# Kernel optimization log

Hardware: AMD Instinct MI355X
Metric: run time of the kernel (lower is better)

The kernel has to match this reference:

```python
import jax, jax.numpy as jnp
import numpy as np
from jax import lax

IN_CH = 64
OUT_CH = 64
K = 3
CW = 2 * IN_CH + 49  # in_ch_weight = 2*in_ch + MAX_DISPLACEMENT**2 = 177
B = 8


def setup_inputs() -> dict:
    key = jax.random.key(0)
    ks = jax.random.split(key, 14)
    f = lambda k, s, sc: jax.random.normal(k, s, dtype=jnp.float32) * sc
    he5 = lambda cin: (2.0 / (cin * 25)) ** 0.5
    he3 = lambda cin: (2.0 / (cin * 9)) ** 0.5
    return {
        "x0": f(ks[0], (B, IN_CH, 128, 160), 1.0),
        "y0": f(ks[1], (B, IN_CH, 128, 160), 1.0),
        "x": f(ks[2], (B, IN_CH, 64, 80), 1.0),
        "y": f(ks[3], (B, IN_CH, 64, 80), 1.0),
        # weight-branch 0 (outputs CW channels)
        "w1a": f(ks[4], (IN_CH, CW, 5, 5), he5(CW)),
        "w1b": f(ks[5], (IN_CH, IN_CH, 5, 5), he5(IN_CH)),
        "w1c": f(ks[6], (CW, IN_CH, 3, 3), he3(IN_CH)),
        # weight-branch 1 / final (outputs OUT_CH channels)
        "w2a": f(ks[7], (IN_CH, CW, 5, 5), he5(CW)),
        "w2b": f(ks[8], (IN_CH, IN_CH, 5, 5), he5(IN_CH)),
        "w2c": f(ks[9], (OUT_CH, IN_CH, 3, 3), he3(IN_CH)),
        # grouped 1x1 dynamic-weight generators (per-channel affine maps)
        "wx_w": f(ks[10], (CW, CW * K * K), 0.05),
        "wx_b": f(ks[11], (CW, CW * K * K), 0.05),
        "wxf_w": f(ks[12], (OUT_CH, OUT_CH * K * K), 0.05),
        "wxf_b": f(ks[13], (OUT_CH, OUT_CH * K * K), 0.05),
    }


def _conv(x, w, stride, pad):
    return lax.conv_general_dilated(
        x, w, (stride, stride), [(pad, pad), (pad, pad)],
        dimension_numbers=("NCHW", "OIHW", "NCHW"))


def _pool2(x):
    b, c, h, w = x.shape
    return x.reshape(b, c, h // 2, 2, w // 2, 2).mean(axis=(3, 5))


def _corr(x0, y0):
    # FlowNet-style correlation: max_displacement=7, stride2=2 ->
    # displacements {-6,-4,-2,0,2,4,6}^2 = 49 channels; mean over C.
    b, c, h, w = x0.shape
    D = 6
    yp = jnp.pad(y0, ((0, 0), (0, 0), (D, D), (D, D)))
    outs = []
    for dy in range(-6, 7, 2):
        for dx in range(-6, 7, 2):
            ys = yp[:, :, D + dy:D + dy + h, D + dx:D + dx + w]
            outs.append(jnp.mean(x0 * ys, axis=1))
    return jnp.stack(outs, axis=1)  # [B, 49, H, W]


def _branch(feat, wa, wb, wc):
    h = jax.nn.relu(_conv(feat, wa, 2, 2))
    h = jax.nn.relu(_conv(h, wb, 2, 2))
    h = _conv(h, wc, 2, 1)
    return h.mean(axis=(2, 3))  # adaptive_avg_pool2d -> (1,1), squeezed: [B, Cout]


def _adaptive_conv(x, w, pad):
    # per-sample conv weights w: [B, Cout, Cin, k, k]
    def one(xb, wb):
        return _conv(xb[None], wb, 1, pad)[0]
    return jax.vmap(one)(x, w)


def reference(x0, y0, x, y, w1a, w1b, w1c, w2a, w2b, w2c, wx_w, wx_b, wxf_w, wxf_b):
    b = x.shape[0]
    x0p = _pool2(x0)
    y0p = _pool2(y0)
    corr = _corr(x0p, y0p)                      # [B, 49, H, W]
    feat = jnp.concatenate([corr, x, y], axis=1)  # [B, CW, H, W]

    # iteration 0 (N-1 = 1): generate per-sample [CW,CW,3,3] filters, apply
    fv = _branch(feat, w1a, w1b, w1c)           # [B, CW]
    wx = (fv[:, :, None] * wx_w[None] + wx_b[None]).reshape(b, CW, CW, K, K)
    feat = jax.nn.relu(_adaptive_conv(feat, wx, K // 2))

    # final: generate per-sample [OUT_CH,OUT_CH,3,3] filters and return them
    fv = _branch(feat, w2a, w2b, w2c)           # [B, OUT_CH]
    wxf = (fv[:, :, None] * wxf_w[None] + wxf_b[None]).reshape(b, OUT_CH, OUT_CH, K, K)
    return wxf
```

## Files before the change

kernel.cpp:

```cpp
#include <hip/hip_runtime.h>

typedef unsigned short u16;
typedef __attribute__((ext_vector_type(8))) short bf16x8;
typedef __attribute__((ext_vector_type(4))) float f32x4;
typedef _Float16 half2_t __attribute__((ext_vector_type(2)));

static constexpr int B  = 8;
static constexpr int C  = 64;
static constexpr int CW = 177;
static constexpr int H  = 64, W  = 80;
static constexpr int HP = 68, WP = 84, KC = 192;
static constexpr int PB = HP * WP * KC;
static constexpr int HA = 36, WA = 44;

__device__ __forceinline__ u16 f2b(float f) {
  union { float f; unsigned u; } v; v.f = f;
  unsigned u = v.u;
  return (u16)((u + 0x7FFF + ((u >> 16) & 1)) >> 16);
}
__device__ __forceinline__ u16 f2h(float f) {
  union { _Float16 h; u16 u; } v; v.h = (_Float16)f; return v.u;
}
__device__ __forceinline__ half2_t h2(unsigned u) {
  union { unsigned u; half2_t h; } v; v.u = u; return v.h;
}
__device__ __forceinline__ float blo(unsigned u) {
  union { unsigned v; float f; } t; t.v = u << 16; return t.f;
}
__device__ __forceinline__ float bhi(unsigned u) {
  union { unsigned v; float f; } t; t.v = u & 0xffff0000u; return t.f;
}
__device__ __forceinline__ unsigned pk2(u16 a, u16 b) {
  return (unsigned)a | ((unsigned)b << 16);
}

__global__ __launch_bounds__(256) void setup_pool(
    const float* __restrict__ x0, const float* __restrict__ y0,
    u16* __restrict__ xpT, u16* __restrict__ ypT,
    const float* __restrict__ w1a, const float* __restrict__ w2a,
    const float* __restrict__ w1b, const float* __restrict__ w2b,
    u16* __restrict__ A5a, u16* __restrict__ A5b,
    u16* __restrict__ A5b1, u16* __restrict__ A5b2,
    u16* __restrict__ featP1, u16* __restrict__ haP, u16* __restrict__ featP2) {
  __shared__ u16 lt[80][66];
  int blk0 = blockIdx.x;
  int tid = threadIdx.x;
  if (blk0 < 1024) {
    int sel = blk0 & 1; int h = (blk0 >> 1) & 63; int b = blk0 >> 7;
    const float* in = sel ? y0 : x0;
    u16* out = sel ? ypT : xpT;
#pragma unroll
    for (int i = 0; i < 20; ++i) {
      int e = i * 256 + tid;
      int c = e / 80, w = e % 80;
      const float* p = in + ((size_t)(b * 64 + c) * 128 + 2 * h) * 160 + 2 * w;
      float2 r0 = *(const float2*)p;
      float2 r1 = *(const float2*)(p + 160);
      lt[w][c] = f2h(0.25f * (r0.x + r0.y + r1.x + r1.y));
    }
    __syncthreads();
#pragma unroll
    for (int i = 0; i < 20; ++i) {
      int e = i * 256 + tid;
      int w = e / 64, c = e % 64;
      out[((size_t)(b * H + h) * W + w) * C + c] = lt[w][c];
    }
    return;
  }
  int idx = (blk0 - 1024) * 256 + tid;
  const int n0r = (B * PB) / 8;
  const int n1r = (B * HA * WA * 64) / 8;
  const int n2r = B * 592 * 24;
  const int s1 = 25 * 64 * 192, s2 = 25 * 64 * 64;
  bf16x8 z = 0;
  if (idx < n0r) { ((bf16x8*)featP1)[idx] = z; return; }
  idx -= n0r;
  if (idx < n1r) { ((bf16x8*)haP)[idx] = z; return; }
  idx -= n1r;
  if (idx < n2r) {
    int ch = idx % 24; int pi = (idx / 24) % 592; int b = idx / (24 * 592);
    int row, col;
    if (pi < 336) { int rr = pi / 84; row = (rr < 2) ? rr : rr + 64; col = pi % 84; }
    else { int pj = pi - 336; row = 2 + (pj >> 2); int cc = pj & 3; col = (cc < 2) ? cc : cc + 80; }
    *(bf16x8*)(featP2 + ((size_t)(b * HP + row) * WP + col) * KC + ch * 8) = z;
    return;
  }
  idx -= n2r;
  if (idx < 2 * s1) {
    const float* w = idx < s1 ? w1a : w2a; u16* A = idx < s1 ? A5a : A5b;
    int e = idx % s1;
    int j = e % 192; int i = (e / 192) % 64; int kk = e / (192 * 64);
    int ky = kk / 5, kx = kk % 5;
    float v = (j < CW) ? w[(((size_t)i * CW + j) * 5 + ky) * 5 + kx] : 0.f;
    A[e] = f2b(v);
    return;
  }
  idx -= 2 * s1;
  if (idx < 2 * s2) {
    const float* w = idx < s2 ? w1b : w2b; u16* A = idx < s2 ? A5b1 : A5b2;
    int e = idx % s2;
    int j = e % 64; int i = (e / 64) % 64; int kk = e / (64 * 64);
    int ky = kk / 5, kx = kk % 5;
    A[e] = f2b(w[(((size_t)i * 64 + j) * 5 + ky) * 5 + kx]);
  }
}

__global__ __launch_bounds__(256) void corr_copy(
    const u16* __restrict__ xpT, const u16* __restrict__ ypT,
    const float* __restrict__ x, const float* __restrict__ y,
    u16* __restrict__ featP) {
  __shared__ float smf[40 * 129];
  int blk0 = blockIdx.x;
  int tid = threadIdx.x;
  if (blk0 < 7840) {
    int b = blk0 & 7; int inner = blk0 >> 3;
    int e = inner * 256 + tid;
    int o = e % 49; int p = e / 49;
    int w = p % W; int h = p / W;
    int dy = (o / 7) * 2 - 6, dx = (o % 7) * 2 - 6;
    int hh = h + dy, ww = w + dx;
    float s = 0.f;
    if (hh >= 0 && hh < H && ww >= 0 && ww < W) {
      const uint4* xv = (const uint4*)(xpT + ((size_t)(b * H + h) * W + w) * C);
      const uint4* yv = (const uint4*)(ypT + ((size_t)(b * H + hh) * W + ww) * C);
#pragma unroll
      for (int i = 0; i < 8; ++i) {
        uint4 a = xv[i], q = yv[i];
        s = __builtin_amdgcn_fdot2(h2(a.x), h2(q.x), s, false);
        s = __builtin_amdgcn_fdot2(h2(a.y), h2(q.y), s, false);
        s = __builtin_amdgcn_fdot2(h2(a.z), h2(q.z), s, false);
        s = __builtin_amdgcn_fdot2(h2(a.w), h2(q.w), s, false);
      }
    }
    s *= (1.0f / 64.0f);
    featP[((size_t)(b * HP + h + 2) * WP + (w + 2)) * KC + o] = f2b(s);
    return;
  }
  int blk = blk0 - 7840;
  float (*lt)[129] = (float(*)[129])smf;
  int half = blk & 1; int h = (blk >> 1) & 63; int b = blk >> 7;
#pragma unroll
  for (int i = 0; i < 20; ++i) {
    int e = i * 256 + tid;
    int c2 = e / 40, w = e % 40;
    const float* src = (c2 < 64) ? x : y;
    int c = c2 & 63;
    lt[w][c2] = src[((size_t)(b * 64 + c) * H + h) * W + half * 40 + w];
  }
  __syncthreads();
#pragma unroll
  for (int i = 0; i < 20; ++i) {
    int e = i * 256 + tid;
    int wr = e / 128, c = e % 128;
    featP[((size_t)(b * HP + h + 2) * WP + (half * 40 + wr + 2)) * KC + 49 + c] = f2b(lt[wr][c]);
  }
}

__global__ void wx_pack(const float* __restrict__ fv, const float* __restrict__ ww,
                        const float* __restrict__ wb, u16* __restrict__ Apk) {
  int idx = blockIdx.x * blockDim.x + threadIdx.x;
  if (idx >= 9 * 192 * 24) return;
  int j8 = idx % 24; int i = (idx / 24) % 192; int kk = idx / (24 * 192);
  float wwv[8], wbv[8];
#pragma unroll
  for (int jj = 0; jj < 8; ++jj) {
    int j = j8 * 8 + jj;
    if (i < CW && j < CW) {
      size_t o = ((size_t)i * CW + j) * 9 + kk;
      wwv[jj] = ww[o]; wbv[jj] = wb[o];
    } else { wwv[jj] = 0.f; wbv[jj] = 0.f; }
  }
  int rb = i >> 4, il = i & 15;
  int c = j8 >> 3, rem = j8 & 7, half = rem >> 2, kqq = rem & 3;
  size_t dst = (((((size_t)kk * 12 + rb) * 3 + c) * 2 + half) * 64 + kqq * 16 + il) * 8;
  for (int b = 0; b < B; ++b) {
    float f = (i < CW) ? fv[b * CW + i] : 0.f;
    u16 o[8];
#pragma unroll
    for (int jj = 0; jj < 8; ++jj) o[jj] = f2b(f * wwv[jj] + wbv[jj]);
    uint4 v; v.x = pk2(o[0], o[1]); v.y = pk2(o[2], o[3]); v.z = pk2(o[4], o[5]); v.w = pk2(o[6], o[7]);
    *(uint4*)(Apk + (size_t)b * 331776 + dst) = v;
  }
}

__global__ __launch_bounds__(256, 2) void ad_conv_kernel(
    const u16* __restrict__ Apk, const u16* __restrict__ featP, u16* __restrict__ outP) {
  __shared__ u16 lds[2][84 * 64];
  int bid = (int)(blockIdx.x % 8) * 64 + (int)(blockIdx.x / 8);
  int h = bid & 63; int b = bid >> 6;
  int tid = threadIdx.x;
  int lane = tid & 63; int wm = tid >> 6;
  int l15 = lane & 15, kq = lane >> 4;

  f32x4 acc[3][5];
#pragma unroll
  for (int i = 0; i < 3; ++i)
#pragma unroll
    for (int j = 0; j < 5; ++j) acc[i][j] = (f32x4){0.f, 0.f, 0.f, 0.f};

  const u16* fb = featP + (size_t)b * PB;
  const u16* Ab = Apk + (size_t)b * 331776 + (size_t)lane * 8;

  int i0 = tid, i1 = tid + 256, i2 = tid + 512;
  int q0 = i0 >> 3, s0 = i0 & 7;
  int q1 = i1 >> 3, s1 = i1 & 7;
  int q2 = i2 >> 3, s2 = i2 & 7;
  int w0 = (i0 * 16) ^ ((q0 & 7) << 4);
  int w1 = (i1 * 16) ^ ((q1 & 7) << 4);
  int w2 = (i2 * 16) ^ ((q2 & 7) << 4);
  bool a2 = i2 < 672;

  bf16x8 r0, r1, r2;
  {
    const u16* g = fb + ((size_t)(h + 1) * WP) * KC;
    r0 = *(const bf16x8*)(g + (size_t)q0 * KC + s0 * 8);
    r1 = *(const bf16x8*)(g + (size_t)q1 * KC + s1 * 8);
    if (a2) r2 = *(const bf16x8*)(g + (size_t)q2 * KC + s2 * 8);
    char* lw = (char*)lds[0];
    *(bf16x8*)(lw + w0) = r0;
    *(bf16x8*)(lw + w1) = r1;
    if (a2) *(bf16x8*)(lw + w2) = r2;
  }
  __syncthreads();

#pragma unroll
  for (int s = 0; s < 9; ++s) {
    const int c = s / 3, ty = s % 3;
    if (s < 8) {
      const int cn = (s + 1) / 3, tyn = (s + 1) % 3;
      const u16* g = fb + ((size_t)(h + 1 + tyn) * WP) * KC + cn * 64;
      r0 = *(const bf16x8*)(g + (size_t)q0 * KC + s0 * 8);
      r1 = *(const bf16x8*)(g + (size_t)q1 * KC + s1 * 8);
      if (a2) r2 = *(const bf16x8*)(g + (size_t)q2 * KC + s2 * 8);
    }
    const char* lb = (const char*)lds[s & 1];
#pragma unroll
    for (int tx = 0; tx < 3; ++tx) {
      const int tap = ty * 3 + tx;
#pragma unroll
      for (int hk = 0; hk < 2; ++hk) {
        bf16x8 av[3], bv[5];
#pragma unroll
        for (int fm = 0; fm < 3; ++fm)
          av[fm] = *(const bf16x8*)(Ab + (size_t)(((tap * 12 + wm * 3 + fm) * 3 + c) * 2 + hk) * 512);
#pragma unroll
        for (int fn = 0; fn < 5; ++fn) {
          int q = fn * 16 + l15 + tx + 1;
          int byte = ((q * 8 + hk * 4 + kq) * 16) ^ ((q & 7) << 4);
          bv[fn] = *(const bf16x8*)(lb + byte);
        }
        __builtin_amdgcn_s_setprio(1);
#pragma unroll
        for (int fm = 0; fm < 3; ++fm)
#pragma unroll
          for (int fn = 0; fn < 5; ++fn)
            acc[fm][fn] = __builtin_amdgcn_mfma_f32_16x16x32_bf16(av[fm], bv[fn], acc[fm][fn], 0, 0, 0);
        __builtin_amdgcn_s_setprio(0);
      }
    }
    if (s < 8) {
      char* lw = (char*)lds[(s + 1) & 1];
      *(bf16x8*)(lw + w0) = r0;
      *(bf16x8*)(lw + w1) = r1;
      if (a2) *(bf16x8*)(lw + w2) = r2;
      __syncthreads();
    }
  }

#pragma unroll
  for (int fm = 0; fm < 3; ++fm) {
    int i0r = wm * 48 + fm * 16 + kq * 4;
#pragma unroll
    for (int fn = 0; fn < 5; ++fn) {
      int ow = fn * 16 + l15;
      u16* dst = outP + ((size_t)(b * HP + h + 2) * WP + (ow + 2)) * KC + i0r;
      uint2 pkv;
      pkv.x = pk2(f2b(fmaxf(acc[fm][fn][0], 0.f)), f2b(fmaxf(acc[fm][fn][1], 0.f)));
      pkv.y = pk2(f2b(fmaxf(acc[fm][fn][2], 0.f)), f2b(fmaxf(acc[fm][fn][3], 0.f)));
      *(uint2*)dst = pkv;
    }
  }
}

__global__ __launch_bounds__(128, 3) void conv5_split_kernel(
    const u16* __restrict__ A5, const u16* __restrict__ featP, u16* __restrict__ pa) {
  __shared__ u16 lds[2][84 * 64];
  int bid = (int)(blockIdx.x % 8) * 160 + (int)(blockIdx.x / 8);
  int rp = bid % 16; int ty = (bid / 16) % 5; int csel = (bid / 80) % 2; int b = bid / 160;
  int r0 = rp * 2;
  int kc0 = csel * 3;
  int tid = threadIdx.x;
  int lane = tid & 63; int wm = tid >> 6;
  int l15 = lane & 15, kq = lane >> 4;

  f32x4 acc[2][5];
#pragma unroll
  for (int i = 0; i < 2; ++i)
#pragma unroll
    for (int j = 0; j < 5; ++j) acc[i][j] = (f32x4){0.f, 0.f, 0.f, 0.f};

  const u16* fb = featP + (size_t)b * PB;
  int rowg0 = 2 * r0 + ty;

  bf16x8 r[6];
  auto load_chunk = [&](int kc) {
#pragma unroll
    for (int it = 0; it < 6; ++it) {
      int idx = it * 128 + tid;
      if (idx < 672) {
        int slot = idx & 3; int q = (idx >> 2) % 84; int row = idx / 336;
        r[it] = *(const bf16x8*)(fb + ((size_t)(rowg0 + 2 * row) * WP + q) * KC + kc * 32 + slot * 8);
      }
    }
  };
  auto write_chunk = [&](int buf) {
    char* lw = (char*)lds[buf];
#pragma unroll
    for (int it = 0; it < 6; ++it) {
      int idx = it * 128 + tid;
      if (idx < 672) {
        int q = (idx >> 2) % 84;
        int byte = (idx * 16) ^ ((q & 7) << 4);
        *(bf16x8*)(lw + byte) = r[it];
      }
    }
  };

  load_chunk(kc0);
  write_chunk(0);
  __syncthreads();

#pragma unroll
  for (int k = 0; k < 3; ++k) {
    int kc = kc0 + k;
    if (k < 2) load_chunk(kc + 1);
    const char* lb = (const char*)lds[k & 1];
#pragma unroll
    for (int tx = 0; tx < 5; ++tx) {
      bf16x8 av[2], bv[5];
#pragma unroll
      for (int fm = 0; fm < 2; ++fm)
        av[fm] = *(const bf16x8*)(A5 + ((size_t)((ty * 5 + tx) * 64 + wm * 32 + fm * 16 + l15)) * 192 + kc * 32 + kq * 8);
#pragma unroll
      for (int fn = 0; fn < 5; ++fn) {
        int p = fn * 16 + l15;
        int orow = p / 40, ocol = p % 40;
        int q = ocol * 2 + tx;
        int byte = (((orow * 84 + q) * 4 + kq) * 16) ^ ((q & 7) << 4);
        bv[fn] = *(const bf16x8*)(lb + byte);
      }
      __builtin_amdgcn_s_setprio(1);
#pragma unroll
      for (int fm = 0; fm < 2; ++fm)
#pragma unroll
        for (int fn = 0; fn < 5; ++fn)
          acc[fm][fn] = __builtin_amdgcn_mfma_f32_16x16x32_bf16(av[fm], bv[fn], acc[fm][fn], 0, 0, 0);
      __builtin_amdgcn_s_setprio(0);
    }
    if (k < 2) {
      write_chunk((k + 1) & 1);
      __syncthreads();
    }
  }
  int slot10 = csel * 5 + ty;
#pragma unroll
  for (int fm = 0; fm < 2; ++fm) {
    int oc0 = wm * 32 + fm * 16 + kq * 4;
#pragma unroll
    for (int fn = 0; fn < 5; ++fn) {
      int p = fn * 16 + l15;
      int orow = r0 + p / 40, ocol = p % 40;
      u16* dst = pa + (((((size_t)slot10 * B + b) * 32 + orow) * 40 + ocol) * 64) + oc0;
      uint2 pkv;
      pkv.x = pk2(f2b(acc[fm][fn][0]), f2b(acc[fm][fn][1]));
      pkv.y = pk2(f2b(acc[fm][fn][2]), f2b(acc[fm][fn][3]));
      *(uint2*)dst = pkv;
    }
  }
}

__global__ void combine10(const u16* __restrict__ pa, u16* __restrict__ haP) {
  int idx = blockIdx.x * blockDim.x + threadIdx.x;
  if (idx >= B * 32 * 40 * 8) return;
  int c8 = idx & 7; int t = idx >> 3;
  int ocol = t % 40; t /= 40; int orow = t % 32; int b = t / 32;
  float s[8];
#pragma unroll
  for (int k = 0; k < 8; ++k) s[k] = 0.f;
#pragma unroll
  for (int sl = 0; sl < 10; ++sl) {
    const u16* p = pa + ((((size_t)sl * B + b) * 32 + orow) * 40 + ocol) * 64 + c8 * 8;
    uint4 v = *(const uint4*)p;
    s[0] += blo(v.x); s[1] += bhi(v.x); s[2] += blo(v.y); s[3] += bhi(v.y);
    s[4] += blo(v.z); s[5] += bhi(v.z); s[6] += blo(v.w); s[7] += bhi(v.w);
  }
  uint4 o;
  o.x = pk2(f2b(fmaxf(s[0], 0.f)), f2b(fmaxf(s[1], 0.f)));
  o.y = pk2(f2b(fmaxf(s[2], 0.f)), f2b(fmaxf(s[3], 0.f)));
  o.z = pk2(f2b(fmaxf(s[4], 0.f)), f2b(fmaxf(s[5], 0.f)));
  o.w = pk2(f2b(fmaxf(s[6], 0.f)), f2b(fmaxf(s[7], 0.f)));
  *(uint4*)(haP + ((size_t)(b * HA + orow + 2) * WA + (ocol + 2)) * 64 + c8 * 8) = o;
}

template<int TY, int TX, int S, int OH, int OW, int M, int BM, int BN, int POFF,
         int KCIN, int HPIN, int WPIN>
__global__ __launch_bounds__(256) void gemm_conv(
    const u16* __restrict__ A, const u16* __restrict__ featP,
    float* __restrict__ outF, int MT, int NT) {
  constexpr int WM = BM / 2, WN = BN / 2, FM = WM / 16, FN = WN / 16;
  constexpr int NKC = KCIN / 32;
  int nwg = gridDim.x;
  int bid = (int)(blockIdx.x % 8) * (nwg / 8) + (int)(blockIdx.x / 8);
  int mt = bid % MT; int rest = bid / MT; int nt = rest % NT; int b = rest / NT;
  int lane = threadIdx.x & 63; int wv = threadIdx.x >> 6;
  int wm = wv >> 1, wn = wv & 1;
  int l15 = lane & 15, kq = lane >> 4;

  f32x4 acc[FM][FN];
#pragma unroll
  for (int i = 0; i < FM; ++i)
#pragma unroll
    for (int j = 0; j < FN; ++j) acc[i][j] = (f32x4){0.f, 0.f, 0.f, 0.f};

  const u16* Abase = A + (size_t)(mt * BM + wm * WM + l15) * KCIN + kq * 8;
  const u16* fb = featP + (size_t)b * (HPIN * WPIN * KCIN) + kq * 8;

  int ohh[FN], oww[FN];
#pragma unroll
  for (int fn = 0; fn < FN; ++fn) {
    int p = nt * BN + wn * WN + fn * 16 + l15;
    ohh[fn] = p / OW; oww[fn] = p % OW;
  }

  for (int kc = 0; kc < NKC; ++kc) {
    for (int ty = 0; ty < TY; ++ty)
      for (int tx = 0; tx < TX; ++tx) {
        const u16* At = Abase + (size_t)((ty * TX + tx) * M) * KCIN + kc * 32;
        bf16x8 av[FM], bv[FN];
#pragma unroll
        for (int fm = 0; fm < FM; ++fm)
          av[fm] = *(const bf16x8*)(At + fm * 16 * KCIN);
#pragma unroll
        for (int fn = 0; fn < FN; ++fn) {
          int hi = ohh[fn] * S + ty + POFF;
          int wi = oww[fn] * S + tx + POFF;
          bv[fn] = *(const bf16x8*)(fb + (size_t)(hi * WPIN + wi) * KCIN + kc * 32);
        }
#pragma unroll
        for (int fm = 0; fm < FM; ++fm)
#pragma unroll
          for (int fn = 0; fn < FN; ++fn)
            acc[fm][fn] = __builtin_amdgcn_mfma_f32_16x16x32_bf16(av[fm], bv[fn], acc[fm][fn], 0, 0, 0);
      }
  }

#pragma unroll
  for (int fm = 0; fm < FM; ++fm) {
    int oc0 = mt * BM + wm * WM + fm * 16 + kq * 4;
#pragma unroll
    for (int fn = 0; fn < FN; ++fn) {
#pragma unroll
      for (int r = 0; r < 4; ++r) {
        float v = fmaxf(acc[fm][fn][r], 0.f);
        outF[(((size_t)b * M + oc0 + r) * OH + ohh[fn]) * OW + oww[fn]] = v;
      }
    }
  }
}

__global__ void tapsum_kernel(const float* __restrict__ hb, float* __restrict__ Sm) {
  int b = blockIdx.x >> 6; int ic = blockIdx.x & 63; int lane = threadIdx.x;
  const float* p = hb + ((size_t)(b * 64 + ic)) * 320;
  float s[9];
#pragma unroll
  for (int t = 0; t < 9; ++t) s[t] = 0.f;
  for (int i = lane; i < 320; i += 64) {
    int ih = i / 20, iw = i % 20;
    float v = p[i];
#pragma unroll
    for (int ky = 0; ky < 3; ++ky) {
      int t2 = ih + 1 - ky;
      if (t2 < 0 || t2 > 14 || (t2 & 1)) continue;
#pragma unroll
      for (int kx = 0; kx < 3; ++kx) {
        int t3 = iw + 1 - kx;
        if (t3 < 0 || t3 > 18 || (t3 & 1)) continue;
        s[ky * 3 + kx] += v;
      }
    }
  }
#pragma unroll
  for (int t = 0; t < 9; ++t)
#pragma unroll
    for (int off = 32; off > 0; off >>= 1) s[t] += __shfl_down(s[t], off);
  if (lane == 0) {
#pragma unroll
    for (int t = 0; t < 9; ++t) Sm[(b * 64 + ic) * 9 + t] = s[t];
  }
}

__global__ void gemv_fv(const float* __restrict__ w3, const float* __restrict__ Sm,
                        float* __restrict__ fv, int OC) {
  int o = blockIdx.x % OC; int b = blockIdx.x / OC; int lane = threadIdx.x;
  const float* wp = w3 + ((size_t)o * 64 + lane) * 9;
  const float* sp = Sm + ((size_t)b * 64 + lane) * 9;
  float acc = 0.f;
#pragma unroll
  for (int t = 0; t < 9; ++t) acc += wp[t] * sp[t];
#pragma unroll
  for (int off = 32; off > 0; off >>= 1) acc += __shfl_down(acc, off);
  if (lane == 0) fv[b * OC + o] = acc * (1.0f / 80.0f);
}

__global__ void gemv_final(const float* __restrict__ w3, const float* __restrict__ Sm,
                           const float* __restrict__ ww, const float* __restrict__ wb,
                           float* __restrict__ out) {
  int o = blockIdx.x & 63; int b = blockIdx.x >> 6; int lane = threadIdx.x;
  const float* wp = w3 + ((size_t)o * 64 + lane) * 9;
  const float* sp = Sm + ((size_t)b * 64 + lane) * 9;
  float acc = 0.f;
#pragma unroll
  for (int t = 0; t < 9; ++t) acc += wp[t] * sp[t];
#pragma unroll
  for (int off = 32; off > 0; off >>= 1) acc += __shfl_down(acc, off);
  float fvv = __shfl(acc, 0) * (1.0f / 80.0f);
  const float* wwp = ww + (size_t)o * 576;
  const float* wbp = wb + (size_t)o * 576;
  float* op = out + ((size_t)(b * 64 + o)) * 576;
#pragma unroll
  for (int k = 0; k < 9; ++k)
    op[k * 64 + lane] = fvv * wwp[k * 64 + lane] + wbp[k * 64 + lane];
}

extern "C" void kernel_launch(void* const* d_in, const int* in_sizes, int n_in,
                              void* d_out, int out_size, void* d_ws, size_t ws_size,
                              hipStream_t stream) {
  const float* x0    = (const float*)d_in[0];
  const float* y0    = (const float*)d_in[1];
  const float* x     = (const float*)d_in[2];
  const float* y     = (const float*)d_in[3];
  const float* w1a   = (const float*)d_in[4];
  const float* w1b   = (const float*)d_in[5];
  const float* w1c   = (const float*)d_in[6];
  const float* w2a   = (const float*)d_in[7];
  const float* w2b   = (const float*)d_in[8];
  const float* w2c   = (const float*)d_in[9];
  const float* wx_w  = (const float*)d_in[10];
  const float* wx_b  = (const float*)d_in[11];
  const float* wxf_w = (const float*)d_in[12];
  const float* wxf_b = (const float*)d_in[13];
  float* out = (float*)d_out;

  char* base = (char*)d_ws;
  size_t off = 0;
  auto take = [&](size_t bytes) -> char* {
    char* p = base + off; off += (bytes + 255) & ~(size_t)255; return p;
  };
  u16*   featP1 = (u16*)take((size_t)B * PB * 2);
  u16*   featP2 = (u16*)take((size_t)B * PB * 2);
  u16*   paAwx  = (u16*)take((size_t)10 * B * 32 * 40 * 64 * 2);
  u16*   pa     = paAwx;
  u16*   Apk    = paAwx;
  u16*   xpT    = paAwx;
  u16*   ypT    = paAwx + (size_t)B * H * W * C;
  u16*   A5a    = (u16*)take((size_t)25 * 64 * 192 * 2);
  u16*   A5b    = (u16*)take((size_t)25 * 64 * 192 * 2);
  u16*   A5b1   = (u16*)take((size_t)25 * 64 * 64 * 2);
  u16*   A5b2   = (u16*)take((size_t)25 * 64 * 64 * 2);
  u16*   haP    = (u16*)take((size_t)B * HA * WA * 64 * 2);
  float* hb     = (float*)take((size_t)B * 64 * 320 * 4);
  float* Sm     = (float*)take((size_t)B * 64 * 9 * 4);
  float* fv1    = (float*)take((size_t)B * CW * 4);
  if (off > ws_size) return;

  const int TB = 256;

  {
    int nsetup = (B * PB) / 8 + (B * HA * WA * 64) / 8 + B * 592 * 24
               + 2 * 25 * 64 * 192 + 2 * 25 * 64 * 64;
    int grid = 1024 + (nsetup + TB - 1) / TB;
    setup_pool<<<grid, TB, 0, stream>>>(x0, y0, xpT, ypT,
        w1a, w2a, w1b, w2b, A5a, A5b, A5b1, A5b2, featP1, haP, featP2);
  }
  corr_copy<<<7840 + 1024, TB, 0, stream>>>(xpT, ypT, x, y, featP1);

  conv5_split_kernel<<<1280, 128, 0, stream>>>(A5a, featP1, pa);
  combine10<<<(B * 32 * 40 * 8 + TB - 1) / TB, TB, 0, stream>>>(pa, haP);
  gemm_conv<5, 5, 2, 16, 20, 64, 32, 32, 0, 64, HA, WA>
      <<<160, TB, 0, stream>>>(A5b1, haP, hb, 2, 10);
  tapsum_kernel<<<B * 64, 64, 0, stream>>>(hb, Sm);
  gemv_fv<<<B * CW, 64, 0, stream>>>(w1c, Sm, fv1, CW);

  wx_pack<<<(9 * 192 * 24 + TB - 1) / TB, TB, 0, stream>>>(fv1, wx_w, wx_b, Apk);
  ad_conv_kernel<<<64 * B, 256, 0, stream>>>(Apk, featP1, featP2);

  conv5_split_kernel<<<1280, 128, 0, stream>>>(A5b, featP2, pa);
  combine10<<<(B * 32 * 40 * 8 + TB - 1) / TB, TB, 0, stream>>>(pa, haP);
  gemm_conv<5, 5, 2, 16, 20, 64, 32, 32, 0, 64, HA, WA>
      <<<160, TB, 0, stream>>>(A5b2, haP, hb, 2, 10);
  tapsum_kernel<<<B * 64, 64, 0, stream>>>(hb, Sm);
  gemv_final<<<B * 64, 64, 0, stream>>>(w2c, Sm, wxf_w, wxf_b, out);
}
```

Baseline: 195.7 us.

## Stage correlation y rows in swizzled LDS and keep x in registers

```diff
diff --git a/kernel.cpp b/kernel.cpp
--- a/kernel.cpp
+++ b/kernel.cpp
@@ -109,35 +109,68 @@
     const u16* __restrict__ xpT, const u16* __restrict__ ypT,
     const float* __restrict__ x, const float* __restrict__ y,
     u16* __restrict__ featP) {
-  __shared__ float smf[40 * 129];
+  __shared__ char sm[40960];
   int blk0 = blockIdx.x;
   int tid = threadIdx.x;
-  if (blk0 < 7840) {
-    int b = blk0 & 7; int inner = blk0 >> 3;
-    int e = inner * 256 + tid;
-    int o = e % 49; int p = e / 49;
-    int w = p % W; int h = p / W;
-    int dy = (o / 7) * 2 - 6, dx = (o % 7) * 2 - 6;
-    int hh = h + dy, ww = w + dx;
-    float s = 0.f;
-    if (hh >= 0 && hh < H && ww >= 0 && ww < W) {
-      const uint4* xv = (const uint4*)(xpT + ((size_t)(b * H + h) * W + w) * C);
-      const uint4* yv = (const uint4*)(ypT + ((size_t)(b * H + hh) * W + ww) * C);
-#pragma unroll
-      for (int i = 0; i < 8; ++i) {
-        uint4 a = xv[i], q = yv[i];
-        s = __builtin_amdgcn_fdot2(h2(a.x), h2(q.x), s, false);
-        s = __builtin_amdgcn_fdot2(h2(a.y), h2(q.y), s, false);
-        s = __builtin_amdgcn_fdot2(h2(a.z), h2(q.z), s, false);
-        s = __builtin_amdgcn_fdot2(h2(a.w), h2(q.w), s, false);
-      }
-    }
-    s *= (1.0f / 64.0f);
-    featP[((size_t)(b * HP + h + 2) * WP + (w + 2)) * KC + o] = f2b(s);
+  if (blk0 < 512) {
+    int b = blk0 & 7; int h = blk0 >> 3;
+    const u16* yb = ypT + (size_t)b * (H * W * C);
+    uint4 xv[8];
+    {
+      const u16* xb = xpT + (((size_t)b * H + h) * W + (tid % 80)) * C;
+#pragma unroll
+      for (int s = 0; s < 8; ++s) xv[s] = *(const uint4*)(xb + s * 8);
+    }
+    int w = tid % 80; int og = tid / 80;
+    u16* dst = featP + ((size_t)(b * HP + h + 2) * WP + (w + 2)) * KC;
+#pragma unroll
+    for (int ph = 0; ph < 2; ++ph) {
+      const int nrows = ph ? 3 : 4;
+      const int nch = nrows * 640;
+      if (ph) __syncthreads();
+      for (int it = 0; it * 256 + tid < nch; ++it) {
+        int idx = it * 256 + tid;
+        int row = idx / 640; int rem = idx - row * 640; int q = rem >> 3; int slot = rem & 7;
+        int hh = h - 6 + 2 * (ph * 4 + row);
+        bf16x8 v = 0;
+        if (hh >= 0 && hh < H) v = *(const bf16x8*)(yb + ((size_t)hh * W + q) * C + slot * 8);
+        int byte = (idx * 16) ^ ((q & 7) << 4);
+        *(bf16x8*)(sm + byte) = v;
+      }
+      __syncthreads();
+      if (tid < 240) {
+        const int base = ph ? 28 : 0;
+        const int cnt = ph ? 7 : 10;
+        const int bound = ph ? 49 : 28;
+#pragma unroll
+        for (int oi = 0; oi < 10; ++oi) {
+          if (oi >= cnt) break;
+          int o = base + og * cnt + oi;
+          if (o < bound) {
+            int rr = o / 7; int dx = (o % 7) * 2 - 6;
+            int lr = rr - ph * 4;
+            int ww = w + dx;
+            float s = 0.f;
+            if (ww >= 0 && ww < W) {
+#pragma unroll
+              for (int sl = 0; sl < 8; ++sl) {
+                int byte = (((lr * 640) + ww * 8 + sl) * 16) ^ ((ww & 7) << 4);
+                uint4 yv = *(const uint4*)(sm + byte);
+                s = __builtin_amdgcn_fdot2(h2(xv[sl].x), h2(yv.x), s, false);
+                s = __builtin_amdgcn_fdot2(h2(xv[sl].y), h2(yv.y), s, false);
+                s = __builtin_amdgcn_fdot2(h2(xv[sl].z), h2(yv.z), s, false);
+                s = __builtin_amdgcn_fdot2(h2(xv[sl].w), h2(yv.w), s, false);
+              }
+            }
+            dst[o] = f2b(s * (1.0f / 64.0f));
+          }
+        }
+      }
+    }
     return;
   }
-  int blk = blk0 - 7840;
-  float (*lt)[129] = (float(*)[129])smf;
+  int blk = blk0 - 512;
+  float (*lt)[129] = (float(*)[129])sm;
   int half = blk & 1; int h = (blk >> 1) & 63; int b = blk >> 7;
 #pragma unroll
   for (int i = 0; i < 20; ++i) {
@@ -582,7 +615,7 @@
     setup_pool<<<grid, TB, 0, stream>>>(x0, y0, xpT, ypT,
         w1a, w2a, w1b, w2b, A5a, A5b, A5b1, A5b2, featP1, haP, featP2);
   }
-  corr_copy<<<7840 + 1024, TB, 0, stream>>>(xpT, ypT, x, y, featP1);
+  corr_copy<<<512 + 1024, TB, 0, stream>>>(xpT, ypT, x, y, featP1);
 
   conv5_split_kernel<<<1280, 128, 0, stream>>>(A5a, featP1, pa);
   combine10<<<(B * 32 * 40 * 8 + TB - 1) / TB, TB, 0, stream>>>(pa, haP);
```

New measurement: 172.7 us, median of 2. 1.13x faster.
